# Optimization experiments

Hardware: AMD Instinct MI355X
Metric: run time of the kernel (lower is better)

Reference implementation:

```python
import jax, jax.numpy as jnp
import numpy as np

D_MODEL = 512
D_FF = 512
N_EXPERTS = 16
TOP_K = 3
BATCH, SEQ = 1, 2048


def setup_inputs() -> dict:
    key = jax.random.key(0)
    ks = jax.random.split(key, 6)
    x = jax.random.normal(ks[0], (BATCH, SEQ, D_MODEL), dtype=jnp.float32)
    # router gate (std=0.01 per _init_weights)
    gate_w = 0.01 * jax.random.normal(ks[1], (N_EXPERTS, D_MODEL), dtype=jnp.float32)
    expert_bias = jnp.zeros((N_EXPERTS,), dtype=jnp.float32)  # registered buffer, zeros
    # shared SwiGLU expert (std=0.02)
    shared_gate_up = 0.02 * jax.random.normal(ks[2], (2 * D_FF, D_MODEL), dtype=jnp.float32)
    shared_down = 0.02 * jax.random.normal(ks[3], (D_MODEL, D_FF), dtype=jnp.float32)
    # batched routed experts (std=0.02)
    expert_gate_up = 0.02 * jax.random.normal(ks[4], (N_EXPERTS, 2 * D_FF, D_MODEL), dtype=jnp.float32)
    expert_down = 0.02 * jax.random.normal(ks[5], (N_EXPERTS, D_MODEL, D_FF), dtype=jnp.float32)
    return {
        "x": x,
        "gate_w": gate_w,
        "expert_bias": expert_bias,
        "shared_gate_up": shared_gate_up,
        "shared_down": shared_down,
        "expert_gate_up": expert_gate_up,
        "expert_down": expert_down,
    }


def _swiglu(combined):
    gate, up = jnp.split(combined, 2, axis=-1)
    return jax.nn.silu(gate) * up


def reference(x, gate_w, expert_bias, shared_gate_up, shared_down, expert_gate_up, expert_down):
    B, S, D = x.shape
    xf = x.reshape(-1, D)  # [T, D]

    # ---- shared expert (always active) ----
    shared_out = _swiglu(xf @ shared_gate_up.T) @ shared_down.T  # [T, D]

    # ---- router: sigmoid affinity + bias-adjusted top-k ----
    logits = xf @ gate_w.T  # [T, E]
    affinity = jax.nn.sigmoid(logits)
    routing_scores = affinity + expert_bias  # expert_bias buffer (zeros)
    _, sel = jax.lax.top_k(routing_scores, TOP_K)  # [T, K]
    sel_aff = jnp.take_along_axis(affinity, sel, axis=1)  # [T, K]
    gating = sel_aff / (sel_aff.sum(axis=-1, keepdims=True) + 1e-9)  # [T, K]

    # ---- routed experts: per-token SwiGLU with the token's expert weights ----
    # Computed densely per expert then gathered; identical math to the
    # per-token weight-gather in BatchedExperts.
    combined = jnp.einsum('td,efd->tef', xf, expert_gate_up)  # [T, E, 2F]
    hidden = _swiglu(combined)  # [T, E, F]
    expert_out = jnp.einsum('tef,edf->ted', hidden, expert_down)  # [T, E, D]
    sel_out = jnp.take_along_axis(expert_out, sel[:, :, None], axis=1)  # [T, K, D]
    routed_out = jnp.einsum('tk,tkd->td', gating, sel_out)  # [T, D]

    out = shared_out + routed_out  # dropout p=0.0 -> identity
    return out.reshape(B, S, D)
```

## Files before the change

### kernel.cpp

```cpp
#include <hip/hip_runtime.h>

#define T_TOK 2048
#define DM    512
#define DFF   512
#define NE    16

typedef __attribute__((ext_vector_type(8))) short bf16x8;
typedef __attribute__((ext_vector_type(4))) float f32x4;
typedef __attribute__((ext_vector_type(8))) unsigned short us8;

__device__ __forceinline__ unsigned short f2bf(float f) {
  unsigned int u = __float_as_uint(f);
  u += 0x7fffu + ((u >> 16) & 1u);
  return (unsigned short)(u >> 16);
}

__device__ __forceinline__ void dma16(const unsigned short* g, unsigned short* l) {
  __builtin_amdgcn_global_load_lds(
      (const __attribute__((address_space(1))) unsigned int*)g,
      (__attribute__((address_space(3))) unsigned int*)l, 16, 0, 0);
}

#define LDSOFF(row, chunk) ((((row) << 7) + ((((chunk) ^ ((row) & 7))) << 4)))

#define MFMA(a,b,c) __builtin_amdgcn_mfma_f32_16x16x32_bf16((a),(b),(c),0,0,0)

__global__ __launch_bounds__(256) void prep_kernel(
    const float* __restrict__ x, const float* __restrict__ gw,
    const float* __restrict__ bias, int* __restrict__ counts,
    int* __restrict__ list, float* __restrict__ wgt,
    const float* __restrict__ sgu, const float* __restrict__ sdn,
    const float* __restrict__ egu, const float* __restrict__ edn,
    unsigned short* __restrict__ xb,   unsigned short* __restrict__ sgub,
    unsigned short* __restrict__ sdnb, unsigned short* __restrict__ egub,
    unsigned short* __restrict__ ednb, float* __restrict__ out)
{
  const int tid = threadIdx.x;
  if (blockIdx.x >= 512) {
    const int cb = blockIdx.x - 512;
    const int ct = cb * 256 + tid;
    const int CT = 7040 * 256;
    const float4 z4 = {0.f, 0.f, 0.f, 0.f};
    for (int i = ct; i < 262144; i += CT) ((float4*)out)[i] = z4;
    int g = ct;
    const float* s; unsigned short* d; int l;
    if      (g <  131072) { s = x;   d = xb;   l = g;           }
    else if (g <  196608) { s = sgu; d = sgub; l = g -  131072; }
    else if (g <  229376) { s = sdn; d = sdnb; l = g -  196608; }
    else if (g < 1277952) { s = egu; d = egub; l = g -  229376; }
    else                  { s = edn; d = ednb; l = g - 1277952; }
    const float* p = s + (size_t)l * 8;
    float4 v0 = *(const float4*)p;
    float4 v1 = *(const float4*)(p + 4);
    us8 o;
    o[0]=f2bf(v0.x); o[1]=f2bf(v0.y); o[2]=f2bf(v0.z); o[3]=f2bf(v0.w);
    o[4]=f2bf(v1.x); o[5]=f2bf(v1.y); o[6]=f2bf(v1.z); o[7]=f2bf(v1.w);
    *(us8*)(d + (size_t)l * 8) = o;
    return;
  }

  __shared__ float lg[4][16];
  __shared__ int bcnt[16], bbase[16];
  __shared__ int sel_s[4][3], pos_s[4][3];
  __shared__ float g_s[4][3];

  const int w = tid >> 6, lane = tid & 63;
  if (tid < 16) bcnt[tid] = 0;
  const int tok = blockIdx.x * 4 + w;
  const int e = lane & 15, part = lane >> 4;

  const float* xr = x + (size_t)tok * DM + part * 128;
  const float* wr = gw + (size_t)e * DM + part * 128;
  float acc = 0.f;
  #pragma unroll 8
  for (int i = 0; i < 128; i += 4) {
    float4 xv = *(const float4*)(xr + i);
    float4 wv = *(const float4*)(wr + i);
    acc += xv.x*wv.x + xv.y*wv.y + xv.z*wv.z + xv.w*wv.w;
  }
  acc += __shfl_xor(acc, 16);
  acc += __shfl_xor(acc, 32);
  if (lane < 16) lg[w][lane] = 1.f / (1.f + __expf(-acc));
  __syncthreads();

  if (tid < 4) {
    float aff[16], sc[16];
    #pragma unroll
    for (int i = 0; i < 16; ++i) { aff[i] = lg[tid][i]; sc[i] = aff[i] + bias[i]; }
    int sel[3]; float sa[3]; float sum = 0.f;
    #pragma unroll
    for (int k = 0; k < 3; ++k) {
      float best = -1e30f; int bi = 0;
      for (int i = 0; i < 16; ++i) {
        bool used = false;
        for (int j = 0; j < k; ++j) used |= (sel[j] == i);
        if (!used && sc[i] > best) { best = sc[i]; bi = i; }
      }
      sel[k] = bi; sa[k] = aff[bi]; sum += aff[bi];
    }
    float inv = 1.f / (sum + 1e-9f);
    #pragma unroll
    for (int k = 0; k < 3; ++k) {
      int p = atomicAdd(&bcnt[sel[k]], 1);
      sel_s[tid][k] = sel[k]; pos_s[tid][k] = p; g_s[tid][k] = sa[k] * inv;
    }
  }
  __syncthreads();
  if (tid < 16) bbase[tid] = atomicAdd(&counts[tid], bcnt[tid]);
  __syncthreads();
  if (tid < 4) {
    #pragma unroll
    for (int k = 0; k < 3; ++k) {
      int E = sel_s[tid][k];
      int p = bbase[E] + pos_s[tid][k];
      list[E * T_TOK + p] = blockIdx.x * 4 + tid;
      wgt [E * T_TOK + p] = g_s[tid][k];
    }
  }
}

__global__ __launch_bounds__(256, 3) void gemm1_fused(
    const unsigned short* __restrict__ X, const unsigned short* __restrict__ Wsh,
    const unsigned short* __restrict__ Wex, unsigned short* __restrict__ Hall,
    const int* __restrict__ counts, const int* __restrict__ list)
{
  __shared__ unsigned short SA[2][64][64];
  __shared__ unsigned short SG[2][64][64];
  __shared__ unsigned short SU[2][64][64];

  const int n0 = blockIdx.x * 64;
  const int mt = blockIdx.y, z = blockIdx.z;
  int cnt, hb; const unsigned short* W;
  if (z == 0) { cnt = T_TOK; hb = 0; W = Wsh; }
  else {
    const int e = z - 1;
    cnt = counts[e];
    if (mt * 64 >= cnt) return;
    hb = T_TOK;
    for (int i = 0; i < e; ++i) hb += counts[i];
    W = Wex + (size_t)e * (2 * DFF * DM);
  }

  const int tid = threadIdx.x, w = tid >> 6, lane = tid & 63;
  const int r0 = w * 16 + (lane >> 3);
  const int cch = (lane & 7) ^ (r0 & 7);
  const unsigned short* ga[2];
  #pragma unroll
  for (int q = 0; q < 2; ++q) {
    int ra = mt * 64 + r0 + q * 8;
    int rc = ra < cnt ? ra : cnt - 1;
    int tokr = (z == 0) ? rc : list[(z - 1) * T_TOK + rc];
    ga[q] = X + (size_t)tokr * DM + cch * 8;
  }
  const unsigned short *gg[2], *gu[2];
  #pragma unroll
  for (int q = 0; q < 2; ++q) {
    int rb = n0 + r0 + q * 8;
    gg[q] = W + (size_t)rb * DM + cch * 8;
    gu[q] = W + (size_t)(DFF + rb) * DM + cch * 8;
  }
  unsigned short* lA[2][2]; unsigned short* lG[2][2]; unsigned short* lU[2][2];
  #pragma unroll
  for (int b = 0; b < 2; ++b)
    #pragma unroll
    for (int q = 0; q < 2; ++q) {
      lA[b][q] = &SA[b][w * 16 + q * 8][0];
      lG[b][q] = &SG[b][w * 16 + q * 8][0];
      lU[b][q] = &SU[b][w * 16 + q * 8][0];
    }

  const int wm = ((tid >> 6) & 1) * 32;
  const int wn = ((tid >> 7) & 1) * 32;
  const int lr = lane & 15, qd = lane >> 4;
  const char* const sa = (const char*)SA;
  const char* const sg = (const char*)SG;
  const char* const su = (const char*)SU;

  const f32x4 z4 = {0.f, 0.f, 0.f, 0.f};
  f32x4 accg[2][2], accu[2][2];
  #pragma unroll
  for (int i = 0; i < 2; ++i)
    #pragma unroll
    for (int j = 0; j < 2; ++j) { accg[i][j] = z4; accu[i][j] = z4; }

  #pragma unroll
  for (int q = 0; q < 2; ++q) {
    dma16(ga[q], lA[0][q]); dma16(gg[q], lG[0][q]); dma16(gu[q], lU[0][q]);
  }

  #pragma unroll
  for (int i = 0; i < DM / 64; ++i) {
    const int b = i & 1;
    __syncthreads();
    if (i + 1 < DM / 64) {
      const int k1 = (i + 1) * 64, nb = b ^ 1;
      #pragma unroll
      for (int q = 0; q < 2; ++q) {
        dma16(ga[q] + k1, lA[nb][q]);
        dma16(gg[q] + k1, lG[nb][q]);
        dma16(gu[q] + k1, lU[nb][q]);
      }
    }
    const int bo = b * 8192;
    #pragma unroll
    for (int ks = 0; ks < 2; ++ks) {
      const int ch = ks * 4 + qd;
      bf16x8 a0 = *(const bf16x8*)(sa + bo + LDSOFF(wm      + lr, ch));
      bf16x8 a1 = *(const bf16x8*)(sa + bo + LDSOFF(wm + 16 + lr, ch));
      bf16x8 g0 = *(const bf16x8*)(sg + bo + LDSOFF(wn      + lr, ch));
      bf16x8 g1 = *(const bf16x8*)(sg + bo + LDSOFF(wn + 16 + lr, ch));
      bf16x8 u0 = *(const bf16x8*)(su + bo + LDSOFF(wn      + lr, ch));
      bf16x8 u1 = *(const bf16x8*)(su + bo + LDSOFF(wn + 16 + lr, ch));
      accg[0][0] = MFMA(a0, g0, accg[0][0]);
      accg[0][1] = MFMA(a0, g1, accg[0][1]);
      accg[1][0] = MFMA(a1, g0, accg[1][0]);
      accg[1][1] = MFMA(a1, g1, accg[1][1]);
      accu[0][0] = MFMA(a0, u0, accu[0][0]);
      accu[0][1] = MFMA(a0, u1, accu[0][1]);
      accu[1][0] = MFMA(a1, u0, accu[1][0]);
      accu[1][1] = MFMA(a1, u1, accu[1][1]);
    }
  }

  #pragma unroll
  for (int sm = 0; sm < 2; ++sm)
    #pragma unroll
    for (int sn = 0; sn < 2; ++sn) {
      const int col = n0 + wn + sn * 16 + lr;
      #pragma unroll
      for (int r = 0; r < 4; ++r) {
        const int ent = mt * 64 + wm + sm * 16 + qd * 4 + r;
        if (ent < cnt) {
          float g = accg[sm][sn][r];
          float u = accu[sm][sn][r];
          float h = (g / (1.f + __expf(-g))) * u;
          Hall[(size_t)(hb + ent) * DFF + col] = f2bf(h);
        }
      }
    }
}

__global__ __launch_bounds__(256, 4) void gemm2_fused(
    const unsigned short* __restrict__ Hall, const unsigned short* __restrict__ Wsh,
    const unsigned short* __restrict__ Wex, float* __restrict__ out,
    const int* __restrict__ counts, const int* __restrict__ list,
    const float* __restrict__ wgt)
{
  __shared__ unsigned short SA[2][64][64];
  __shared__ unsigned short SB[2][64][64];

  const int n0 = blockIdx.x * 64;
  const int mt = blockIdx.y, z = blockIdx.z;
  int cnt, hb; const unsigned short* W;
  if (z == 0) { cnt = T_TOK; hb = 0; W = Wsh; }
  else {
    const int e = z - 1;
    cnt = counts[e];
    if (mt * 64 >= cnt) return;
    hb = T_TOK;
    for (int i = 0; i < e; ++i) hb += counts[i];
    W = Wex + (size_t)e * (DM * DFF);
  }

  const int tid = threadIdx.x, w = tid >> 6, lane = tid & 63;
  const int r0 = w * 16 + (lane >> 3);
  const int cch = (lane & 7) ^ (r0 & 7);
  const unsigned short* ga[2];
  #pragma unroll
  for (int q = 0; q < 2; ++q) {
    int ra = mt * 64 + r0 + q * 8;
    int rc = ra < cnt ? ra : cnt - 1;
    ga[q] = Hall + (size_t)(hb + rc) * DFF + cch * 8;
  }
  const unsigned short* gb[2];
  #pragma unroll
  for (int q = 0; q < 2; ++q)
    gb[q] = W + (size_t)(n0 + r0 + q * 8) * DFF + cch * 8;
  unsigned short* lA[2][2]; unsigned short* lB[2][2];
  #pragma unroll
  for (int b = 0; b < 2; ++b)
    #pragma unroll
    for (int q = 0; q < 2; ++q) {
      lA[b][q] = &SA[b][w * 16 + q * 8][0];
      lB[b][q] = &SB[b][w * 16 + q * 8][0];
    }

  const int wm = ((tid >> 6) & 1) * 32;
  const int wn = ((tid >> 7) & 1) * 32;
  const int lr = lane & 15, qd = lane >> 4;
  const char* const sa = (const char*)SA;
  const char* const sb = (const char*)SB;

  const f32x4 z4 = {0.f, 0.f, 0.f, 0.f};
  f32x4 acc[2][2];
  #pragma unroll
  for (int i = 0; i < 2; ++i)
    #pragma unroll
    for (int j = 0; j < 2; ++j) acc[i][j] = z4;

  #pragma unroll
  for (int q = 0; q < 2; ++q) { dma16(ga[q], lA[0][q]); dma16(gb[q], lB[0][q]); }

  #pragma unroll
  for (int i = 0; i < DFF / 64; ++i) {
    const int b = i & 1;
    __syncthreads();
    if (i + 1 < DFF / 64) {
      const int k1 = (i + 1) * 64, nb = b ^ 1;
      #pragma unroll
      for (int q = 0; q < 2; ++q) {
        dma16(ga[q] + k1, lA[nb][q]);
        dma16(gb[q] + k1, lB[nb][q]);
      }
    }
    const int bo = b * 8192;
    #pragma unroll
    for (int ks = 0; ks < 2; ++ks) {
      const int ch = ks * 4 + qd;
      bf16x8 a0 = *(const bf16x8*)(sa + bo + LDSOFF(wm      + lr, ch));
      bf16x8 a1 = *(const bf16x8*)(sa + bo + LDSOFF(wm + 16 + lr, ch));
      bf16x8 b0 = *(const bf16x8*)(sb + bo + LDSOFF(wn      + lr, ch));
      bf16x8 b1 = *(const bf16x8*)(sb + bo + LDSOFF(wn + 16 + lr, ch));
      acc[0][0] = MFMA(a0, b0, acc[0][0]);
      acc[0][1] = MFMA(a0, b1, acc[0][1]);
      acc[1][0] = MFMA(a1, b0, acc[1][0]);
      acc[1][1] = MFMA(a1, b1, acc[1][1]);
    }
  }

  #pragma unroll
  for (int sm = 0; sm < 2; ++sm)
    #pragma unroll
    for (int sn = 0; sn < 2; ++sn) {
      const int col = n0 + wn + sn * 16 + lr;
      #pragma unroll
      for (int r = 0; r < 4; ++r) {
        const int ent = mt * 64 + wm + sm * 16 + qd * 4 + r;
        if (ent < cnt) {
          float v = acc[sm][sn][r];
          if (z == 0) {
            atomicAdd(out + (size_t)ent * DM + col, v);
          } else {
            const int   tok = list[(z - 1) * T_TOK + ent];
            const float g   = wgt [(z - 1) * T_TOK + ent];
            atomicAdd(out + (size_t)tok * DM + col, g * v);
          }
        }
      }
    }
}

extern "C" void kernel_launch(void* const* d_in, const int* in_sizes, int n_in,
                              void* d_out, int out_size, void* d_ws, size_t ws_size,
                              hipStream_t stream) {
  const float* x    = (const float*)d_in[0];
  const float* gw   = (const float*)d_in[1];
  const float* bias = (const float*)d_in[2];
  const float* sgu  = (const float*)d_in[3];
  const float* sdn  = (const float*)d_in[4];
  const float* egu  = (const float*)d_in[5];
  const float* edn  = (const float*)d_in[6];
  float* out = (float*)d_out;

  char* ws = (char*)d_ws;
  int*            counts = (int*)(ws + 0);
  int*            list   = (int*)(ws + 64);
  float*          wgt    = (float*)(ws + 131136);
  unsigned short* Hall   = (unsigned short*)(ws + 262208);
  unsigned short* xb     = (unsigned short*)(ws + 8650816);
  unsigned short* sgub   = (unsigned short*)(ws + 10747968);
  unsigned short* sdnb   = (unsigned short*)(ws + 11796544);
  unsigned short* egub   = (unsigned short*)(ws + 12320832);
  unsigned short* ednb   = (unsigned short*)(ws + 29098048);
  const size_t need = 37486656;
  if (ws_size < need) return;

  hipMemsetAsync(counts, 0, 64, stream);
  prep_kernel<<<512 + 7040, 256, 0, stream>>>(
      x, gw, bias, counts, list, wgt, sgu, sdn, egu, edn,
      xb, sgub, sdnb, egub, ednb, out);
  gemm1_fused<<<dim3(8, 32, NE + 1), 256, 0, stream>>>(xb, sgub, egub, Hall, counts, list);
  gemm2_fused<<<dim3(8, 32, NE + 1), 256, 0, stream>>>(Hall, sdnb, ednb, out, counts, list, wgt);
}
```

Before: 169.5 us.

## Triple-buffer LDS tiles with explicit vmcnt waits in both expert GEMMs

Both GEMM kernels move from a double-buffered LDS pipeline guarded by __syncthreads to a three-stage ring. The kernels prefetch two K-tiles ahead and wait on global-to-LDS loads with explicit s_waitcnt vmcnt counts before a raw s_barrier. MFMA blocks are also wrapped in s_setprio to favour matrix issue. The extra LDS per block lowers the occupancy targets in launch_bounds (3→2 and 4→3), trading fewer resident blocks for deeper latency hiding.

```diff
diff --git a/kernel.cpp b/kernel.cpp
--- a/kernel.cpp
+++ b/kernel.cpp
@@ -119,14 +119,14 @@
   }
 }
 
-__global__ __launch_bounds__(256, 3) void gemm1_fused(
+__global__ __launch_bounds__(256, 2) void gemm1_fused(
     const unsigned short* __restrict__ X, const unsigned short* __restrict__ Wsh,
     const unsigned short* __restrict__ Wex, unsigned short* __restrict__ Hall,
     const int* __restrict__ counts, const int* __restrict__ list)
 {
-  __shared__ unsigned short SA[2][64][64];
-  __shared__ unsigned short SG[2][64][64];
-  __shared__ unsigned short SU[2][64][64];
+  __shared__ unsigned short SA[3][64][64];
+  __shared__ unsigned short SG[3][64][64];
+  __shared__ unsigned short SU[3][64][64];
 
   const int n0 = blockIdx.x * 64;
   const int mt = blockIdx.y, z = blockIdx.z;
@@ -159,9 +159,9 @@
     gg[q] = W + (size_t)rb * DM + cch * 8;
     gu[q] = W + (size_t)(DFF + rb) * DM + cch * 8;
   }
-  unsigned short* lA[2][2]; unsigned short* lG[2][2]; unsigned short* lU[2][2];
-  #pragma unroll
-  for (int b = 0; b < 2; ++b)
+  unsigned short* lA[3][2]; unsigned short* lG[3][2]; unsigned short* lU[3][2];
+  #pragma unroll
+  for (int b = 0; b < 3; ++b)
     #pragma unroll
     for (int q = 0; q < 2; ++q) {
       lA[b][q] = &SA[b][w * 16 + q * 8][0];
@@ -187,21 +187,28 @@
   for (int q = 0; q < 2; ++q) {
     dma16(ga[q], lA[0][q]); dma16(gg[q], lG[0][q]); dma16(gu[q], lU[0][q]);
   }
-
-  #pragma unroll
-  for (int i = 0; i < DM / 64; ++i) {
-    const int b = i & 1;
-    __syncthreads();
-    if (i + 1 < DM / 64) {
-      const int k1 = (i + 1) * 64, nb = b ^ 1;
+  __builtin_amdgcn_sched_barrier(0);
+  #pragma unroll
+  for (int q = 0; q < 2; ++q) {
+    dma16(ga[q] + 64, lA[1][q]); dma16(gg[q] + 64, lG[1][q]); dma16(gu[q] + 64, lU[1][q]);
+  }
+
+  #pragma unroll
+  for (int t = 0; t < DM / 64; ++t) {
+    if (t < DM / 64 - 1) asm volatile("s_waitcnt vmcnt(6)" ::: "memory");
+    else                 asm volatile("s_waitcnt vmcnt(0)" ::: "memory");
+    __builtin_amdgcn_sched_barrier(0);
+    __builtin_amdgcn_s_barrier();
+    if (t + 2 < DM / 64) {
+      const int nb = (t + 2) % 3, k2 = (t + 2) * 64;
       #pragma unroll
       for (int q = 0; q < 2; ++q) {
-        dma16(ga[q] + k1, lA[nb][q]);
-        dma16(gg[q] + k1, lG[nb][q]);
-        dma16(gu[q] + k1, lU[nb][q]);
+        dma16(ga[q] + k2, lA[nb][q]);
+        dma16(gg[q] + k2, lG[nb][q]);
+        dma16(gu[q] + k2, lU[nb][q]);
       }
     }
-    const int bo = b * 8192;
+    const int bo = (t % 3) * 8192;
     #pragma unroll
     for (int ks = 0; ks < 2; ++ks) {
       const int ch = ks * 4 + qd;
@@ -211,6 +218,7 @@
       bf16x8 g1 = *(const bf16x8*)(sg + bo + LDSOFF(wn + 16 + lr, ch));
       bf16x8 u0 = *(const bf16x8*)(su + bo + LDSOFF(wn      + lr, ch));
       bf16x8 u1 = *(const bf16x8*)(su + bo + LDSOFF(wn + 16 + lr, ch));
+      __builtin_amdgcn_s_setprio(1);
       accg[0][0] = MFMA(a0, g0, accg[0][0]);
       accg[0][1] = MFMA(a0, g1, accg[0][1]);
       accg[1][0] = MFMA(a1, g0, accg[1][0]);
@@ -219,6 +227,7 @@
       accu[0][1] = MFMA(a0, u1, accu[0][1]);
       accu[1][0] = MFMA(a1, u0, accu[1][0]);
       accu[1][1] = MFMA(a1, u1, accu[1][1]);
+      __builtin_amdgcn_s_setprio(0);
     }
   }
 
@@ -240,14 +249,14 @@
     }
 }
 
-__global__ __launch_bounds__(256, 4) void gemm2_fused(
+__global__ __launch_bounds__(256, 3) void gemm2_fused(
     const unsigned short* __restrict__ Hall, const unsigned short* __restrict__ Wsh,
     const unsigned short* __restrict__ Wex, float* __restrict__ out,
     const int* __restrict__ counts, const int* __restrict__ list,
     const float* __restrict__ wgt)
 {
-  __shared__ unsigned short SA[2][64][64];
-  __shared__ unsigned short SB[2][64][64];
+  __shared__ unsigned short SA[3][64][64];
+  __shared__ unsigned short SB[3][64][64];
 
   const int n0 = blockIdx.x * 64;
   const int mt = blockIdx.y, z = blockIdx.z;
@@ -276,9 +285,9 @@
   #pragma unroll
   for (int q = 0; q < 2; ++q)
     gb[q] = W + (size_t)(n0 + r0 + q * 8) * DFF + cch * 8;
-  unsigned short* lA[2][2]; unsigned short* lB[2][2];
-  #pragma unroll
-  for (int b = 0; b < 2; ++b)
+  unsigned short* lA[3][2]; unsigned short* lB[3][2];
+  #pragma unroll
+  for (int b = 0; b < 3; ++b)
     #pragma unroll
     for (int q = 0; q < 2; ++q) {
       lA[b][q] = &SA[b][w * 16 + q * 8][0];
@@ -300,20 +309,25 @@
 
   #pragma unroll
   for (int q = 0; q < 2; ++q) { dma16(ga[q], lA[0][q]); dma16(gb[q], lB[0][q]); }
-
-  #pragma unroll
-  for (int i = 0; i < DFF / 64; ++i) {
-    const int b = i & 1;
-    __syncthreads();
-    if (i + 1 < DFF / 64) {
-      const int k1 = (i + 1) * 64, nb = b ^ 1;
+  __builtin_amdgcn_sched_barrier(0);
+  #pragma unroll
+  for (int q = 0; q < 2; ++q) { dma16(ga[q] + 64, lA[1][q]); dma16(gb[q] + 64, lB[1][q]); }
+
+  #pragma unroll
+  for (int t = 0; t < DFF / 64; ++t) {
+    if (t < DFF / 64 - 1) asm volatile("s_waitcnt vmcnt(4)" ::: "memory");
+    else                  asm volatile("s_waitcnt vmcnt(0)" ::: "memory");
+    __builtin_amdgcn_sched_barrier(0);
+    __builtin_amdgcn_s_barrier();
+    if (t + 2 < DFF / 64) {
+      const int nb = (t + 2) % 3, k2 = (t + 2) * 64;
       #pragma unroll
       for (int q = 0; q < 2; ++q) {
-        dma16(ga[q] + k1, lA[nb][q]);
-        dma16(gb[q] + k1, lB[nb][q]);
+        dma16(ga[q] + k2, lA[nb][q]);
+        dma16(gb[q] + k2, lB[nb][q]);
       }
     }
-    const int bo = b * 8192;
+    const int bo = (t % 3) * 8192;
     #pragma unroll
     for (int ks = 0; ks < 2; ++ks) {
       const int ch = ks * 4 + qd;
@@ -321,10 +335,12 @@
       bf16x8 a1 = *(const bf16x8*)(sa + bo + LDSOFF(wm + 16 + lr, ch));
       bf16x8 b0 = *(const bf16x8*)(sb + bo + LDSOFF(wn      + lr, ch));
       bf16x8 b1 = *(const bf16x8*)(sb + bo + LDSOFF(wn + 16 + lr, ch));
+      __builtin_amdgcn_s_setprio(1);
       acc[0][0] = MFMA(a0, b0, acc[0][0]);
       acc[0][1] = MFMA(a0, b1, acc[0][1]);
       acc[1][0] = MFMA(a1, b0, acc[1][0]);
       acc[1][1] = MFMA(a1, b1, acc[1][1]);
+      __builtin_amdgcn_s_setprio(0);
     }
   }
 
```

New measurement: 173.6 us. +2.4%, slower.

## Merge prep and both GEMMs into one persistent cooperative kernel with grid syncs

Applied to the files above, without the earlier changes.

Replaces the three separate launches (router/convert, gate-up GEMM, down GEMM) with a single cooperative kernel of 512 persistent blocks that uses grid-wide syncs between phases and loops over the former grid tiles. The aim is to remove launch overhead and inter-kernel gaps. In exchange, the grid shrinks to 512 blocks with occupancy limited to 2 per CU, which may lower latency hiding. Every block iterates over all tile indices even when many expert tiles are empty.

```diff
diff --git a/kernel.cpp b/kernel.cpp
--- a/kernel.cpp
+++ b/kernel.cpp
@@ -1,4 +1,7 @@
 #include <hip/hip_runtime.h>
+#include <hip/hip_cooperative_groups.h>
+
+namespace cg = cooperative_groups;
 
 #define T_TOK 2048
 #define DM    512
@@ -25,329 +28,339 @@
 
 #define MFMA(a,b,c) __builtin_amdgcn_mfma_f32_16x16x32_bf16((a),(b),(c),0,0,0)
 
-__global__ __launch_bounds__(256) void prep_kernel(
+struct RouterS {
+  float lg[4][16];
+  int bcnt[16], bbase[16];
+  int sel_s[4][3], pos_s[4][3];
+  float g_s[4][3];
+};
+
+__global__ __launch_bounds__(256, 2) void moe_all(
     const float* __restrict__ x, const float* __restrict__ gw,
-    const float* __restrict__ bias, int* __restrict__ counts,
-    int* __restrict__ list, float* __restrict__ wgt,
+    const float* __restrict__ bias,
     const float* __restrict__ sgu, const float* __restrict__ sdn,
     const float* __restrict__ egu, const float* __restrict__ edn,
-    unsigned short* __restrict__ xb,   unsigned short* __restrict__ sgub,
-    unsigned short* __restrict__ sdnb, unsigned short* __restrict__ egub,
-    unsigned short* __restrict__ ednb, float* __restrict__ out)
+    int* __restrict__ counts, int* __restrict__ list, float* __restrict__ wgt,
+    unsigned short* __restrict__ Hall, unsigned short* __restrict__ xb,
+    unsigned short* __restrict__ sgub, unsigned short* __restrict__ sdnb,
+    unsigned short* __restrict__ egub, unsigned short* __restrict__ ednb,
+    float* __restrict__ out)
 {
+  __shared__ __align__(1024) char smem[49152];
+  const int bid = threadIdx.y * 0 + blockIdx.x;
   const int tid = threadIdx.x;
-  if (blockIdx.x >= 512) {
-    const int cb = blockIdx.x - 512;
-    const int ct = cb * 256 + tid;
-    const int CT = 7040 * 256;
+  const int w = tid >> 6, lane = tid & 63;
+  cg::grid_group grid = cg::this_grid();
+
+  {
+    RouterS& R = *(RouterS*)smem;
+    if (tid < 16) R.bcnt[tid] = 0;
+    const int tok = bid * 4 + w;
+    const int e = lane & 15, part = lane >> 4;
+
+    const float* xr = x + (size_t)tok * DM + part * 128;
+    const float* wr = gw + (size_t)e * DM + part * 128;
+    float acc = 0.f;
+    #pragma unroll 8
+    for (int i = 0; i < 128; i += 4) {
+      float4 xv = *(const float4*)(xr + i);
+      float4 wv = *(const float4*)(wr + i);
+      acc += xv.x*wv.x + xv.y*wv.y + xv.z*wv.z + xv.w*wv.w;
+    }
+    acc += __shfl_xor(acc, 16);
+    acc += __shfl_xor(acc, 32);
+    if (lane < 16) R.lg[w][lane] = 1.f / (1.f + __expf(-acc));
+    __syncthreads();
+
+    if (tid < 4) {
+      float aff[16], sc[16];
+      #pragma unroll
+      for (int i = 0; i < 16; ++i) { aff[i] = R.lg[tid][i]; sc[i] = aff[i] + bias[i]; }
+      int sel[3]; float sa[3]; float sum = 0.f;
+      #pragma unroll
+      for (int k = 0; k < 3; ++k) {
+        float best = -1e30f; int bi = 0;
+        for (int i = 0; i < 16; ++i) {
+          bool used = false;
+          for (int j = 0; j < k; ++j) used |= (sel[j] == i);
+          if (!used && sc[i] > best) { best = sc[i]; bi = i; }
+        }
+        sel[k] = bi; sa[k] = aff[bi]; sum += aff[bi];
+      }
+      float inv = 1.f / (sum + 1e-9f);
+      #pragma unroll
+      for (int k = 0; k < 3; ++k) {
+        int p = atomicAdd(&R.bcnt[sel[k]], 1);
+        R.sel_s[tid][k] = sel[k]; R.pos_s[tid][k] = p; R.g_s[tid][k] = sa[k] * inv;
+      }
+    }
+    __syncthreads();
+    if (tid < 16) R.bbase[tid] = atomicAdd(&counts[tid], R.bcnt[tid]);
+    __syncthreads();
+    if (tid < 4) {
+      #pragma unroll
+      for (int k = 0; k < 3; ++k) {
+        int E = R.sel_s[tid][k];
+        int p = R.bbase[E] + R.pos_s[tid][k];
+        list[E * T_TOK + p] = bid * 4 + tid;
+        wgt [E * T_TOK + p] = R.g_s[tid][k];
+      }
+    }
+
+    const int gidx = bid * 256 + tid;
     const float4 z4 = {0.f, 0.f, 0.f, 0.f};
-    for (int i = ct; i < 262144; i += CT) ((float4*)out)[i] = z4;
-    int g = ct;
-    const float* s; unsigned short* d; int l;
-    if      (g <  131072) { s = x;   d = xb;   l = g;           }
-    else if (g <  196608) { s = sgu; d = sgub; l = g -  131072; }
-    else if (g <  229376) { s = sdn; d = sdnb; l = g -  196608; }
-    else if (g < 1277952) { s = egu; d = egub; l = g -  229376; }
-    else                  { s = edn; d = ednb; l = g - 1277952; }
-    const float* p = s + (size_t)l * 8;
-    float4 v0 = *(const float4*)p;
-    float4 v1 = *(const float4*)(p + 4);
-    us8 o;
-    o[0]=f2bf(v0.x); o[1]=f2bf(v0.y); o[2]=f2bf(v0.z); o[3]=f2bf(v0.w);
-    o[4]=f2bf(v1.x); o[5]=f2bf(v1.y); o[6]=f2bf(v1.z); o[7]=f2bf(v1.w);
-    *(us8*)(d + (size_t)l * 8) = o;
-    return;
+    ((float4*)out)[gidx] = z4;
+    ((float4*)out)[gidx + 131072] = z4;
+
+    #pragma unroll
+    for (int i = 0; i < 14; ++i) {
+      const int g = gidx + i * 131072;
+      if (g < 1802240) {
+        const float* s; unsigned short* d; int l;
+        if      (g <  131072) { s = x;   d = xb;   l = g;           }
+        else if (g <  196608) { s = sgu; d = sgub; l = g -  131072; }
+        else if (g <  229376) { s = sdn; d = sdnb; l = g -  196608; }
+        else if (g < 1277952) { s = egu; d = egub; l = g -  229376; }
+        else                  { s = edn; d = ednb; l = g - 1277952; }
+        const float* p = s + (size_t)l * 8;
+        float4 v0 = *(const float4*)p;
+        float4 v1 = *(const float4*)(p + 4);
+        us8 o;
+        o[0]=f2bf(v0.x); o[1]=f2bf(v0.y); o[2]=f2bf(v0.z); o[3]=f2bf(v0.w);
+        o[4]=f2bf(v1.x); o[5]=f2bf(v1.y); o[6]=f2bf(v1.z); o[7]=f2bf(v1.w);
+        *(us8*)(d + (size_t)l * 8) = o;
+      }
+    }
   }
 
-  __shared__ float lg[4][16];
-  __shared__ int bcnt[16], bbase[16];
-  __shared__ int sel_s[4][3], pos_s[4][3];
-  __shared__ float g_s[4][3];
-
-  const int w = tid >> 6, lane = tid & 63;
-  if (tid < 16) bcnt[tid] = 0;
-  const int tok = blockIdx.x * 4 + w;
-  const int e = lane & 15, part = lane >> 4;
-
-  const float* xr = x + (size_t)tok * DM + part * 128;
-  const float* wr = gw + (size_t)e * DM + part * 128;
-  float acc = 0.f;
-  #pragma unroll 8
-  for (int i = 0; i < 128; i += 4) {
-    float4 xv = *(const float4*)(xr + i);
-    float4 wv = *(const float4*)(wr + i);
-    acc += xv.x*wv.x + xv.y*wv.y + xv.z*wv.z + xv.w*wv.w;
+  __threadfence();
+  grid.sync();
+  __threadfence();
+
+  {
+    char* const sa = smem;
+    char* const sg = smem + 16384;
+    char* const su = smem + 32768;
+    const int r0 = w * 16 + (lane >> 3);
+    const int cch = (lane & 7) ^ (r0 & 7);
+    const int wm = ((tid >> 6) & 1) * 32;
+    const int wn = ((tid >> 7) & 1) * 32;
+    const int lr = lane & 15, qd = lane >> 4;
+
+    for (int v = bid; v < 8 * 32 * (NE + 1); v += 512) {
+      const int bx = v & 7, mt = (v >> 3) & 31, z = v >> 8;
+      const int n0 = bx * 64;
+      int cnt, hb; const unsigned short* W;
+      if (z == 0) { cnt = T_TOK; hb = 0; W = sgub; }
+      else {
+        const int e = z - 1;
+        cnt = counts[e];
+        if (mt * 64 >= cnt) continue;
+        hb = T_TOK;
+        for (int i = 0; i < e; ++i) hb += counts[i];
+        W = egub + (size_t)e * (2 * DFF * DM);
+      }
+
+      const unsigned short* ga[2];
+      #pragma unroll
+      for (int q = 0; q < 2; ++q) {
+        int ra = mt * 64 + r0 + q * 8;
+        int rc = ra < cnt ? ra : cnt - 1;
+        int tokr = (z == 0) ? rc : list[(z - 1) * T_TOK + rc];
+        ga[q] = xb + (size_t)tokr * DM + cch * 8;
+      }
+      const unsigned short *gg[2], *gu[2];
+      #pragma unroll
+      for (int q = 0; q < 2; ++q) {
+        int rb = n0 + r0 + q * 8;
+        gg[q] = W + (size_t)rb * DM + cch * 8;
+        gu[q] = W + (size_t)(DFF + rb) * DM + cch * 8;
+      }
+      unsigned short* lA[2][2]; unsigned short* lG[2][2]; unsigned short* lU[2][2];
+      #pragma unroll
+      for (int b = 0; b < 2; ++b)
+        #pragma unroll
+        for (int q = 0; q < 2; ++q) {
+          const int ro = (w * 16 + q * 8) * 64;
+          lA[b][q] = (unsigned short*)(sa + b * 8192) + ro;
+          lG[b][q] = (unsigned short*)(sg + b * 8192) + ro;
+          lU[b][q] = (unsigned short*)(su + b * 8192) + ro;
+        }
+
+      const f32x4 z4 = {0.f, 0.f, 0.f, 0.f};
+      f32x4 accg[2][2], accu[2][2];
+      #pragma unroll
+      for (int i = 0; i < 2; ++i)
+        #pragma unroll
+        for (int j = 0; j < 2; ++j) { accg[i][j] = z4; accu[i][j] = z4; }
+
+      #pragma unroll
+      for (int q = 0; q < 2; ++q) {
+        dma16(ga[q], lA[0][q]); dma16(gg[q], lG[0][q]); dma16(gu[q], lU[0][q]);
+      }
+
+      #pragma unroll
+      for (int i = 0; i < DM / 64; ++i) {
+        const int b = i & 1;
+        __syncthreads();
+        if (i + 1 < DM / 64) {
+          const int k1 = (i + 1) * 64, nb = b ^ 1;
+          #pragma unroll
+          for (int q = 0; q < 2; ++q) {
+            dma16(ga[q] + k1, lA[nb][q]);
+            dma16(gg[q] + k1, lG[nb][q]);
+            dma16(gu[q] + k1, lU[nb][q]);
+          }
+        }
+        const int bo = b * 8192;
+        #pragma unroll
+        for (int ks = 0; ks < 2; ++ks) {
+          const int ch = ks * 4 + qd;
+          bf16x8 a0 = *(const bf16x8*)(sa + bo + LDSOFF(wm      + lr, ch));
+          bf16x8 a1 = *(const bf16x8*)(sa + bo + LDSOFF(wm + 16 + lr, ch));
+          bf16x8 g0 = *(const bf16x8*)(sg + bo + LDSOFF(wn      + lr, ch));
+          bf16x8 g1 = *(const bf16x8*)(sg + bo + LDSOFF(wn + 16 + lr, ch));
+          bf16x8 u0 = *(const bf16x8*)(su + bo + LDSOFF(wn      + lr, ch));
+          bf16x8 u1 = *(const bf16x8*)(su + bo + LDSOFF(wn + 16 + lr, ch));
+          accg[0][0] = MFMA(a0, g0, accg[0][0]);
+          accg[0][1] = MFMA(a0, g1, accg[0][1]);
+          accg[1][0] = MFMA(a1, g0, accg[1][0]);
+          accg[1][1] = MFMA(a1, g1, accg[1][1]);
+          accu[0][0] = MFMA(a0, u0, accu[0][0]);
+          accu[0][1] = MFMA(a0, u1, accu[0][1]);
+          accu[1][0] = MFMA(a1, u0, accu[1][0]);
+          accu[1][1] = MFMA(a1, u1, accu[1][1]);
+        }
+      }
+      __syncthreads();
+
+      #pragma unroll
+      for (int sm = 0; sm < 2; ++sm)
+        #pragma unroll
+        for (int sn = 0; sn < 2; ++sn) {
+          const int col = n0 + wn + sn * 16 + lr;
+          #pragma unroll
+          for (int r = 0; r < 4; ++r) {
+            const int ent = mt * 64 + wm + sm * 16 + qd * 4 + r;
+            if (ent < cnt) {
+              float g = accg[sm][sn][r];
+              float u = accu[sm][sn][r];
+              float h = (g / (1.f + __expf(-g))) * u;
+              Hall[(size_t)(hb + ent) * DFF + col] = f2bf(h);
+            }
+          }
+        }
+    }
   }
-  acc += __shfl_xor(acc, 16);
-  acc += __shfl_xor(acc, 32);
-  if (lane < 16) lg[w][lane] = 1.f / (1.f + __expf(-acc));
-  __syncthreads();
-
-  if (tid < 4) {
-    float aff[16], sc[16];
-    #pragma unroll
-    for (int i = 0; i < 16; ++i) { aff[i] = lg[tid][i]; sc[i] = aff[i] + bias[i]; }
-    int sel[3]; float sa[3]; float sum = 0.f;
-    #pragma unroll
-    for (int k = 0; k < 3; ++k) {
-      float best = -1e30f; int bi = 0;
-      for (int i = 0; i < 16; ++i) {
-        bool used = false;
-        for (int j = 0; j < k; ++j) used |= (sel[j] == i);
-        if (!used && sc[i] > best) { best = sc[i]; bi = i; }
-      }
-      sel[k] = bi; sa[k] = aff[bi]; sum += aff[bi];
-    }
-    float inv = 1.f / (sum + 1e-9f);
-    #pragma unroll
-    for (int k = 0; k < 3; ++k) {
-      int p = atomicAdd(&bcnt[sel[k]], 1);
-      sel_s[tid][k] = sel[k]; pos_s[tid][k] = p; g_s[tid][k] = sa[k] * inv;
+
+  __threadfence();
+  grid.sync();
+  __threadfence();
+
+  {
+    char* const sa = smem;
+    char* const sb = smem + 16384;
+    const int r0 = w * 16 + (lane >> 3);
+    const int cch = (lane & 7) ^ (r0 & 7);
+    const int wm = ((tid >> 6) & 1) * 32;
+    const int wn = ((tid >> 7) & 1) * 32;
+    const int lr = lane & 15, qd = lane >> 4;
+
+    for (int v = bid; v < 8 * 32 * (NE + 1); v += 512) {
+      const int bx = v & 7, mt = (v >> 3) & 31, z = v >> 8;
+      const int n0 = bx * 64;
+      int cnt, hb; const unsigned short* W;
+      if (z == 0) { cnt = T_TOK; hb = 0; W = sdnb; }
+      else {
+        const int e = z - 1;
+        cnt = counts[e];
+        if (mt * 64 >= cnt) continue;
+        hb = T_TOK;
+        for (int i = 0; i < e; ++i) hb += counts[i];
+        W = ednb + (size_t)e * (DM * DFF);
+      }
+
+      const unsigned short* ga[2];
+      #pragma unroll
+      for (int q = 0; q < 2; ++q) {
+        int ra = mt * 64 + r0 + q * 8;
+        int rc = ra < cnt ? ra : cnt - 1;
+        ga[q] = Hall + (size_t)(hb + rc) * DFF + cch * 8;
+      }
+      const unsigned short* gb[2];
+      #pragma unroll
+      for (int q = 0; q < 2; ++q)
+        gb[q] = W + (size_t)(n0 + r0 + q * 8) * DFF + cch * 8;
+      unsigned short* lA[2][2]; unsigned short* lB[2][2];
+      #pragma unroll
+      for (int b = 0; b < 2; ++b)
+        #pragma unroll
+        for (int q = 0; q < 2; ++q) {
+          const int ro = (w * 16 + q * 8) * 64;
+          lA[b][q] = (unsigned short*)(sa + b * 8192) + ro;
+          lB[b][q] = (unsigned short*)(sb + b * 8192) + ro;
+        }
+
+      const f32x4 z4 = {0.f, 0.f, 0.f, 0.f};
+      f32x4 acc[2][2];
+      #pragma unroll
+      for (int i = 0; i < 2; ++i)
+        #pragma unroll
+        for (int j = 0; j < 2; ++j) acc[i][j] = z4;
+
+      #pragma unroll
+      for (int q = 0; q < 2; ++q) { dma16(ga[q], lA[0][q]); dma16(gb[q], lB[0][q]); }
+
+      #pragma unroll
+      for (int i = 0; i < DFF / 64; ++i) {
+        const int b = i & 1;
+        __syncthreads();
+        if (i + 1 < DFF / 64) {
+          const int k1 = (i + 1) * 64, nb = b ^ 1;
+          #pragma unroll
+          for (int q = 0; q < 2; ++q) {
+            dma16(ga[q] + k1, lA[nb][q]);
+            dma16(gb[q] + k1, lB[nb][q]);
+          }
+        }
+        const int bo = b * 8192;
+        #pragma unroll
+        for (int ks = 0; ks < 2; ++ks) {
+          const int ch = ks * 4 + qd;
+          bf16x8 a0 = *(const bf16x8*)(sa + bo + LDSOFF(wm      + lr, ch));
+          bf16x8 a1 = *(const bf16x8*)(sa + bo + LDSOFF(wm + 16 + lr, ch));
+          bf16x8 b0 = *(const bf16x8*)(sb + bo + LDSOFF(wn      + lr, ch));
+          bf16x8 b1 = *(const bf16x8*)(sb + bo + LDSOFF(wn + 16 + lr, ch));
+          acc[0][0] = MFMA(a0, b0, acc[0][0]);
+          acc[0][1] = MFMA(a0, b1, acc[0][1]);
+          acc[1][0] = MFMA(a1, b0, acc[1][0]);
+          acc[1][1] = MFMA(a1, b1, acc[1][1]);
+        }
+      }
+      __syncthreads();
+
+      #pragma unroll
+      for (int sm = 0; sm < 2; ++sm)
+        #pragma unroll
+        for (int sn = 0; sn < 2; ++sn) {
+          const int col = n0 + wn + sn * 16 + lr;
+          #pragma unroll
+          for (int r = 0; r < 4; ++r) {
+            const int ent = mt * 64 + wm + sm * 16 + qd * 4 + r;
+            if (ent < cnt) {
+              float vv = acc[sm][sn][r];
+              if (z == 0) {
+                atomicAdd(out + (size_t)ent * DM + col, vv);
+              } else {
+                const int   tok = list[(z - 1) * T_TOK + ent];
+                const float gg  = wgt [(z - 1) * T_TOK + ent];
+                atomicAdd(out + (size_t)tok * DM + col, gg * vv);
+              }
+            }
+          }
+        }
     }
   }
-  __syncthreads();
-  if (tid < 16) bbase[tid] = atomicAdd(&counts[tid], bcnt[tid]);
-  __syncthreads();
-  if (tid < 4) {
-    #pragma unroll
-    for (int k = 0; k < 3; ++k) {
-      int E = sel_s[tid][k];
-      int p = bbase[E] + pos_s[tid][k];
-      list[E * T_TOK + p] = blockIdx.x * 4 + tid;
-      wgt [E * T_TOK + p] = g_s[tid][k];
-    }
-  }
-}
-
-__global__ __launch_bounds__(256, 3) void gemm1_fused(
-    const unsigned short* __restrict__ X, const unsigned short* __restrict__ Wsh,
-    const unsigned short* __restrict__ Wex, unsigned short* __restrict__ Hall,
-    const int* __restrict__ counts, const int* __restrict__ list)
-{
-  __shared__ unsigned short SA[2][64][64];
-  __shared__ unsigned short SG[2][64][64];
-  __shared__ unsigned short SU[2][64][64];
-
-  const int n0 = blockIdx.x * 64;
-  const int mt = blockIdx.y, z = blockIdx.z;
-  int cnt, hb; const unsigned short* W;
-  if (z == 0) { cnt = T_TOK; hb = 0; W = Wsh; }
-  else {
-    const int e = z - 1;
-    cnt = counts[e];
-    if (mt * 64 >= cnt) return;
-    hb = T_TOK;
-    for (int i = 0; i < e; ++i) hb += counts[i];
-    W = Wex + (size_t)e * (2 * DFF * DM);
-  }
-
-  const int tid = threadIdx.x, w = tid >> 6, lane = tid & 63;
-  const int r0 = w * 16 + (lane >> 3);
-  const int cch = (lane & 7) ^ (r0 & 7);
-  const unsigned short* ga[2];
-  #pragma unroll
-  for (int q = 0; q < 2; ++q) {
-    int ra = mt * 64 + r0 + q * 8;
-    int rc = ra < cnt ? ra : cnt - 1;
-    int tokr = (z == 0) ? rc : list[(z - 1) * T_TOK + rc];
-    ga[q] = X + (size_t)tokr * DM + cch * 8;
-  }
-  const unsigned short *gg[2], *gu[2];
-  #pragma unroll
-  for (int q = 0; q < 2; ++q) {
-    int rb = n0 + r0 + q * 8;
-    gg[q] = W + (size_t)rb * DM + cch * 8;
-    gu[q] = W + (size_t)(DFF + rb) * DM + cch * 8;
-  }
-  unsigned short* lA[2][2]; unsigned short* lG[2][2]; unsigned short* lU[2][2];
-  #pragma unroll
-  for (int b = 0; b < 2; ++b)
-    #pragma unroll
-    for (int q = 0; q < 2; ++q) {
-      lA[b][q] = &SA[b][w * 16 + q * 8][0];
-      lG[b][q] = &SG[b][w * 16 + q * 8][0];
-      lU[b][q] = &SU[b][w * 16 + q * 8][0];
-    }
-
-  const int wm = ((tid >> 6) & 1) * 32;
-  const int wn = ((tid >> 7) & 1) * 32;
-  const int lr = lane & 15, qd = lane >> 4;
-  const char* const sa = (const char*)SA;
-  const char* const sg = (const char*)SG;
-  const char* const su = (const char*)SU;
-
-  const f32x4 z4 = {0.f, 0.f, 0.f, 0.f};
-  f32x4 accg[2][2], accu[2][2];
-  #pragma unroll
-  for (int i = 0; i < 2; ++i)
-    #pragma unroll
-    for (int j = 0; j < 2; ++j) { accg[i][j] = z4; accu[i][j] = z4; }
-
-  #pragma unroll
-  for (int q = 0; q < 2; ++q) {
-    dma16(ga[q], lA[0][q]); dma16(gg[q], lG[0][q]); dma16(gu[q], lU[0][q]);
-  }
-
-  #pragma unroll
-  for (int i = 0; i < DM / 64; ++i) {
-    const int b = i & 1;
-    __syncthreads();
-    if (i + 1 < DM / 64) {
-      const int k1 = (i + 1) * 64, nb = b ^ 1;
-      #pragma unroll
-      for (int q = 0; q < 2; ++q) {
-        dma16(ga[q] + k1, lA[nb][q]);
-        dma16(gg[q] + k1, lG[nb][q]);
-        dma16(gu[q] + k1, lU[nb][q]);
-      }
-    }
-    const int bo = b * 8192;
-    #pragma unroll
-    for (int ks = 0; ks < 2; ++ks) {
-      const int ch = ks * 4 + qd;
-      bf16x8 a0 = *(const bf16x8*)(sa + bo + LDSOFF(wm      + lr, ch));
-      bf16x8 a1 = *(const bf16x8*)(sa + bo + LDSOFF(wm + 16 + lr, ch));
-      bf16x8 g0 = *(const bf16x8*)(sg + bo + LDSOFF(wn      + lr, ch));
-      bf16x8 g1 = *(const bf16x8*)(sg + bo + LDSOFF(wn + 16 + lr, ch));
-      bf16x8 u0 = *(const bf16x8*)(su + bo + LDSOFF(wn      + lr, ch));
-      bf16x8 u1 = *(const bf16x8*)(su + bo + LDSOFF(wn + 16 + lr, ch));
-      accg[0][0] = MFMA(a0, g0, accg[0][0]);
-      accg[0][1] = MFMA(a0, g1, accg[0][1]);
-      accg[1][0] = MFMA(a1, g0, accg[1][0]);
-      accg[1][1] = MFMA(a1, g1, accg[1][1]);
-      accu[0][0] = MFMA(a0, u0, accu[0][0]);
-      accu[0][1] = MFMA(a0, u1, accu[0][1]);
-      accu[1][0] = MFMA(a1, u0, accu[1][0]);
-      accu[1][1] = MFMA(a1, u1, accu[1][1]);
-    }
-  }
-
-  #pragma unroll
-  for (int sm = 0; sm < 2; ++sm)
-    #pragma unroll
-    for (int sn = 0; sn < 2; ++sn) {
-      const int col = n0 + wn + sn * 16 + lr;
-      #pragma unroll
-      for (int r = 0; r < 4; ++r) {
-        const int ent = mt * 64 + wm + sm * 16 + qd * 4 + r;
-        if (ent < cnt) {
-          float g = accg[sm][sn][r];
-          float u = accu[sm][sn][r];
-          float h = (g / (1.f + __expf(-g))) * u;
-          Hall[(size_t)(hb + ent) * DFF + col] = f2bf(h);
-        }
-      }
-    }
-}
-
-__global__ __launch_bounds__(256, 4) void gemm2_fused(
-    const unsigned short* __restrict__ Hall, const unsigned short* __restrict__ Wsh,
-    const unsigned short* __restrict__ Wex, float* __restrict__ out,
-    const int* __restrict__ counts, const int* __restrict__ list,
-    const float* __restrict__ wgt)
-{
-  __shared__ unsigned short SA[2][64][64];
-  __shared__ unsigned short SB[2][64][64];
-
-  const int n0 = blockIdx.x * 64;
-  const int mt = blockIdx.y, z = blockIdx.z;
-  int cnt, hb; const unsigned short* W;
-  if (z == 0) { cnt = T_TOK; hb = 0; W = Wsh; }
-  else {
-    const int e = z - 1;
-    cnt = counts[e];
-    if (mt * 64 >= cnt) return;
-    hb = T_TOK;
-    for (int i = 0; i < e; ++i) hb += counts[i];
-    W = Wex + (size_t)e * (DM * DFF);
-  }
-
-  const int tid = threadIdx.x, w = tid >> 6, lane = tid & 63;
-  const int r0 = w * 16 + (lane >> 3);
-  const int cch = (lane & 7) ^ (r0 & 7);
-  const unsigned short* ga[2];
-  #pragma unroll
-  for (int q = 0; q < 2; ++q) {
-    int ra = mt * 64 + r0 + q * 8;
-    int rc = ra < cnt ? ra : cnt - 1;
-    ga[q] = Hall + (size_t)(hb + rc) * DFF + cch * 8;
-  }
-  const unsigned short* gb[2];
-  #pragma unroll
-  for (int q = 0; q < 2; ++q)
-    gb[q] = W + (size_t)(n0 + r0 + q * 8) * DFF + cch * 8;
-  unsigned short* lA[2][2]; unsigned short* lB[2][2];
-  #pragma unroll
-  for (int b = 0; b < 2; ++b)
-    #pragma unroll
-    for (int q = 0; q < 2; ++q) {
-      lA[b][q] = &SA[b][w * 16 + q * 8][0];
-      lB[b][q] = &SB[b][w * 16 + q * 8][0];
-    }
-
-  const int wm = ((tid >> 6) & 1) * 32;
-  const int wn = ((tid >> 7) & 1) * 32;
-  const int lr = lane & 15, qd = lane >> 4;
-  const char* const sa = (const char*)SA;
-  const char* const sb = (const char*)SB;
-
-  const f32x4 z4 = {0.f, 0.f, 0.f, 0.f};
-  f32x4 acc[2][2];
-  #pragma unroll
-  for (int i = 0; i < 2; ++i)
-    #pragma unroll
-    for (int j = 0; j < 2; ++j) acc[i][j] = z4;
-
-  #pragma unroll
-  for (int q = 0; q < 2; ++q) { dma16(ga[q], lA[0][q]); dma16(gb[q], lB[0][q]); }
-
-  #pragma unroll
-  for (int i = 0; i < DFF / 64; ++i) {
-    const int b = i & 1;
-    __syncthreads();
-    if (i + 1 < DFF / 64) {
-      const int k1 = (i + 1) * 64, nb = b ^ 1;
-      #pragma unroll
-      for (int q = 0; q < 2; ++q) {
-        dma16(ga[q] + k1, lA[nb][q]);
-        dma16(gb[q] + k1, lB[nb][q]);
-      }
-    }
-    const int bo = b * 8192;
-    #pragma unroll
-    for (int ks = 0; ks < 2; ++ks) {
-      const int ch = ks * 4 + qd;
-      bf16x8 a0 = *(const bf16x8*)(sa + bo + LDSOFF(wm      + lr, ch));
-      bf16x8 a1 = *(const bf16x8*)(sa + bo + LDSOFF(wm + 16 + lr, ch));
-      bf16x8 b0 = *(const bf16x8*)(sb + bo + LDSOFF(wn      + lr, ch));
-      bf16x8 b1 = *(const bf16x8*)(sb + bo + LDSOFF(wn + 16 + lr, ch));
-      acc[0][0] = MFMA(a0, b0, acc[0][0]);
-      acc[0][1] = MFMA(a0, b1, acc[0][1]);
-      acc[1][0] = MFMA(a1, b0, acc[1][0]);
-      acc[1][1] = MFMA(a1, b1, acc[1][1]);
-    }
-  }
-
-  #pragma unroll
-  for (int sm = 0; sm < 2; ++sm)
-    #pragma unroll
-    for (int sn = 0; sn < 2; ++sn) {
-      const int col = n0 + wn + sn * 16 + lr;
-      #pragma unroll
-      for (int r = 0; r < 4; ++r) {
-        const int ent = mt * 64 + wm + sm * 16 + qd * 4 + r;
-        if (ent < cnt) {
-          float v = acc[sm][sn][r];
-          if (z == 0) {
-            atomicAdd(out + (size_t)ent * DM + col, v);
-          } else {
-            const int   tok = list[(z - 1) * T_TOK + ent];
-            const float g   = wgt [(z - 1) * T_TOK + ent];
-            atomicAdd(out + (size_t)tok * DM + col, g * v);
-          }
-        }
-      }
-    }
 }
 
 extern "C" void kernel_launch(void* const* d_in, const int* in_sizes, int n_in,
@@ -376,9 +389,13 @@
   if (ws_size < need) return;
 
   hipMemsetAsync(counts, 0, 64, stream);
-  prep_kernel<<<512 + 7040, 256, 0, stream>>>(
-      x, gw, bias, counts, list, wgt, sgu, sdn, egu, edn,
-      xb, sgub, sdnb, egub, ednb, out);
-  gemm1_fused<<<dim3(8, 32, NE + 1), 256, 0, stream>>>(xb, sgub, egub, Hall, counts, list);
-  gemm2_fused<<<dim3(8, 32, NE + 1), 256, 0, stream>>>(Hall, sdnb, ednb, out, counts, list, wgt);
+
+  void* args[] = {
+    (void*)&x, (void*)&gw, (void*)&bias, (void*)&sgu, (void*)&sdn,
+    (void*)&egu, (void*)&edn, (void*)&counts, (void*)&list, (void*)&wgt,
+    (void*)&Hall, (void*)&xb, (void*)&sgub, (void*)&sdnb, (void*)&egub,
+    (void*)&ednb, (void*)&out
+  };
+  hipLaunchCooperativeKernel((const void*)moe_all, dim3(512), dim3(256),
+                             args, 0, stream);
 }
```

Result: slower. 595.7 us (+251.5%).
